# Kernel optimization log

Measured on AMD Instinct MI355X. Metric: run time of the kernel, lower is better.

Reference implementation:

```python
import jax, jax.numpy as jnp
import numpy as np

B, S, E, H = 2, 2048, 1024, 16
DH = E // H            # 64 head dim
ROT = DH // 2          # 32: RotaryEmbedding(head_dim//2) rotates first 32 dims only
CTX = 2048             # sliding KV window
THETA = 10000.0


def setup_inputs() -> dict:
    key = jax.random.key(0)
    ks = jax.random.split(key, 7)
    sc = 1.0 / np.sqrt(E)
    mk = lambda k, sh, s=1.0: (jax.random.normal(k, sh, jnp.float32) * s)
    return {
        "query": mk(ks[0], (B, S, E)),
        "key":   mk(ks[1], (B, S, E)),
        "value": mk(ks[2], (B, S, E)),
        "Wq": mk(ks[3], (E, E), sc), "bq": jnp.zeros((E,), jnp.float32),
        "Wk": mk(ks[4], (E, E), sc), "bk": jnp.zeros((E,), jnp.float32),
        "Wv": mk(ks[5], (E, E), sc), "bv": jnp.zeros((E,), jnp.float32),
        "Wo": mk(ks[6], (E, E), sc), "bo": jnp.zeros((E,), jnp.float32),
    }


def _rope(t):
    # t: [B, H, S, DH]; rotate first ROT dims, pass the rest through (offset=0).
    seq = t.shape[2]
    inv_freq = 1.0 / (THETA ** (jnp.arange(0, ROT, 2, dtype=jnp.float32) / ROT))  # [ROT//2]
    ang = jnp.arange(seq, dtype=jnp.float32)[:, None] * inv_freq[None, :]          # [S, ROT//2]
    cos = jnp.repeat(jnp.cos(ang), 2, axis=-1)  # [S, ROT] (pairwise-interleaved freqs)
    sin = jnp.repeat(jnp.sin(ang), 2, axis=-1)
    rot, rest = t[..., :ROT], t[..., ROT:]
    x1, x2 = rot[..., 0::2], rot[..., 1::2]
    rot_half = jnp.stack([-x2, x1], axis=-1).reshape(rot.shape)  # rotate_half on pairs
    return jnp.concatenate([rot * cos + rot_half * sin, rest], axis=-1)


def reference(query, key, value, Wq, bq, Wk, bk, Wv, bv, Wo, bo):
    def heads(x, W, b):
        return (x @ W.T + b).reshape(B, -1, H, DH).transpose(0, 2, 1, 3)  # [B,H,S,DH]

    q = _rope(heads(query, Wq, bq))
    k = _rope(heads(key, Wk, bk))
    v = heads(value, Wv, bv)
    k, v = k[:, :, -CTX:], v[:, :, -CTX:]  # sliding window (no-op when S == CTX)

    scale = jnp.float32(1.0 / np.sqrt(DH))
    scores = jnp.einsum('bhqd,bhkd->bhqk', q, k) * scale  # [B,H,Sq,Sk]
    sq, sk = q.shape[2], k.shape[2]
    causal = jnp.tril(jnp.ones((sk, sk), dtype=bool))[-sq:]  # [Sq,Sk]
    scores = jnp.where(causal[None, None], scores, jnp.float32(-jnp.inf))
    probs = jax.nn.softmax(scores, axis=-1)  # dropout=0 (eval)
    out = jnp.einsum('bhqk,bhkd->bhqd', probs, v)
    out = out.transpose(0, 2, 1, 3).reshape(B, -1, E)
    return out @ Wo.T + bo
```

## Files before the change

kernel.cpp:

```cpp
#include <hip/hip_runtime.h>
#include <stdint.h>
#include <math.h>

typedef __bf16 bf16x8 __attribute__((ext_vector_type(8)));
typedef float f32x4 __attribute__((ext_vector_type(4)));

__device__ __forceinline__ float bf2f(uint16_t x) {
  unsigned u = ((unsigned)x) << 16;
  float f;
  __builtin_memcpy(&f, &u, 4);
  return f;
}
__device__ __forceinline__ uint16_t f2bf(float f) {
  __bf16 h = (__bf16)f;
  uint16_t u;
  __builtin_memcpy(&u, &h, 2);
  return u;
}
__device__ __forceinline__ bf16x8 cvt8(const float* p) {
  const float4 lo = *(const float4*)p;
  const float4 hi = *(const float4*)(p + 4);
  bf16x8 v;
  v[0] = (__bf16)lo.x; v[1] = (__bf16)lo.y; v[2] = (__bf16)lo.z; v[3] = (__bf16)lo.w;
  v[4] = (__bf16)hi.x; v[5] = (__bf16)hi.y; v[6] = (__bf16)hi.z; v[7] = (__bf16)hi.w;
  return v;
}

typedef __attribute__((address_space(1))) const unsigned int gu32;
typedef __attribute__((address_space(3))) unsigned int lu32;
__device__ __forceinline__ void async_copy16(const void* gp, void* lp) {
  __builtin_amdgcn_global_load_lds((gu32*)gp, (lu32*)lp, 16, 0, 0);
}

__global__ __launch_bounds__(256) void cvt_kernel(
    const float* __restrict__ s0, uint16_t* __restrict__ d0,
    const float* __restrict__ s1, uint16_t* __restrict__ d1,
    const float* __restrict__ s2, uint16_t* __restrict__ d2) {
  const int z = blockIdx.z;
  const float* s = z == 0 ? s0 : z == 1 ? s1 : s2;
  uint16_t* d = z == 0 ? d0 : z == 1 ? d1 : d2;
  const size_t idx = ((size_t)blockIdx.x * 256 + threadIdx.x) * 8;
  *(bf16x8*)(d + idx) = cvt8(s + idx);
}

template <bool A_F32, bool W_F32, bool C_F32, bool VT, bool ROPE>
__global__ __launch_bounds__(256) void gemm3_kernel(
    const void* __restrict__ A0, const void* __restrict__ W0,
    const float* __restrict__ b0, void* __restrict__ C0,
    const void* __restrict__ A1, const void* __restrict__ W1,
    const float* __restrict__ b1, void* __restrict__ C1,
    const void* __restrict__ A2, const void* __restrict__ W2,
    const float* __restrict__ b2, void* __restrict__ C2,
    int M, int N, int K) {
  const int z = blockIdx.z;
  const void* Av = z == 0 ? A0 : z == 1 ? A1 : A2;
  const void* Wp = z == 0 ? W0 : z == 1 ? W1 : W2;
  const float* bias = z == 0 ? b0 : z == 1 ? b1 : b2;
  void* Cv = z == 0 ? C0 : z == 1 ? C1 : C2;

  __shared__ __align__(16) uint16_t As[128 * 64];
  __shared__ __align__(16) uint16_t Bs[64 * 64];
  const int tid = threadIdx.x;
  const int wave = tid >> 6, lane = tid & 63;
  const int quad = lane >> 4, l16 = lane & 15;
  const int l = blockIdx.y * 16 + blockIdx.x;
  const int bm = (l & 31) << 7;
  const int bn = (l >> 5) << 6;
  const int wm = (wave >> 1) << 6;
  const int wn = (wave & 1) << 5;

  f32x4 acc[4][2] = {};

  for (int k0 = 0; k0 < K; k0 += 64) {
    bf16x8 ar[4], wr[2];
    if (A_F32) {
#pragma unroll
      for (int i = 0; i < 4; i++) {
        const int c = i * 256 + tid;
        const int r = c >> 3, pc = ((c & 7) ^ (r & 7)) << 3;
        ar[i] = cvt8((const float*)Av + (size_t)(bm + r) * K + k0 + pc);
      }
    }
    if (W_F32) {
#pragma unroll
      for (int i = 0; i < 2; i++) {
        const int c = i * 256 + tid;
        const int r = c >> 3, pc = ((c & 7) ^ (r & 7)) << 3;
        wr[i] = cvt8((const float*)Wp + (size_t)(bn + r) * K + k0 + pc);
      }
    }
    if (k0) __syncthreads();
#pragma unroll
    for (int i = 0; i < 4; i++) {
      const int c = i * 256 + tid;
      const int r = c >> 3, pc = ((c & 7) ^ (r & 7)) << 3;
      if (A_F32) *(bf16x8*)(As + c * 8) = ar[i];
      else async_copy16((const uint16_t*)Av + (size_t)(bm + r) * K + k0 + pc,
                        As + (i * 256 + (tid & 192)) * 8);
    }
#pragma unroll
    for (int i = 0; i < 2; i++) {
      const int c = i * 256 + tid;
      const int r = c >> 3, pc = ((c & 7) ^ (r & 7)) << 3;
      if (W_F32) *(bf16x8*)(Bs + c * 8) = wr[i];
      else async_copy16((const uint16_t*)Wp + (size_t)(bn + r) * K + k0 + pc,
                        Bs + (i * 256 + (tid & 192)) * 8);
    }
    __syncthreads();
#pragma unroll
    for (int s = 0; s < 2; s++) {
      bf16x8 af[4], bfr[2];
#pragma unroll
      for (int i = 0; i < 4; i++) {
        const int Ra = wm + i * 16 + l16;
        af[i] = *(const bf16x8*)(As + Ra * 64 + (((s * 4 + quad) ^ (Ra & 7)) << 3));
      }
#pragma unroll
      for (int j = 0; j < 2; j++) {
        const int Rb = wn + j * 16 + l16;
        bfr[j] = *(const bf16x8*)(Bs + Rb * 64 + (((s * 4 + quad) ^ (Rb & 7)) << 3));
      }
#pragma unroll
      for (int i = 0; i < 4; i++)
#pragma unroll
        for (int j = 0; j < 2; j++)
          acc[i][j] = __builtin_amdgcn_mfma_f32_16x16x32_bf16(af[i], bfr[j], acc[i][j], 0, 0, 0);
    }
  }
  if (VT && z == 2) {
#pragma unroll
    for (int j = 0; j < 2; j++) {
      const int n = bn + wn + j * 16 + l16;
      const float bj = bias[n];
      const int h = n >> 6, dh = n & 63;
#pragma unroll
      for (int i = 0; i < 4; i++) {
        const int m0 = bm + wm + i * 16 + quad * 4;
        const int b = m0 >> 11, s0 = m0 & 2047;
        uint2 pk;
        pk.x = (unsigned)f2bf(acc[i][j][0] + bj) |
               ((unsigned)f2bf(acc[i][j][1] + bj) << 16);
        pk.y = (unsigned)f2bf(acc[i][j][2] + bj) |
               ((unsigned)f2bf(acc[i][j][3] + bj) << 16);
        *(uint2*)((uint16_t*)Cv + ((size_t)((b * 16 + h) * 64 + dh)) * 2048 + s0) = pk;
      }
    }
  } else {
#pragma unroll
    for (int j = 0; j < 2; j++) {
      const int n = bn + wn + j * 16 + l16;
      const float bj = bias[n];
      const int dh = wn + j * 16 + l16;
      const bool rot = ROPE && (wn == 0);
      float invrev = 0.f;
      if (rot)
        invrev = __expf(-0.5756462732485115f * (float)(dh >> 1)) *
                 0.15915494309189535f;
#pragma unroll
      for (int i = 0; i < 4; i++) {
        const int m0 = bm + wm + i * 16 + quad * 4;
#pragma unroll
        for (int r = 0; r < 4; r++) {
          float v = acc[i][j][r] + bj;
          if (rot) {
            const int s_pos = (m0 + r) & 2047;
            float rev = (float)s_pos * invrev;
            rev -= floorf(rev);
            const float sn = __builtin_amdgcn_sinf(rev);
            const float cs = __builtin_amdgcn_cosf(rev);
            const float partner = __shfl_xor(v, 1);
            v = (dh & 1) ? (v * cs + partner * sn) : (v * cs - partner * sn);
          }
          if (C_F32) ((float*)Cv)[(size_t)(m0 + r) * N + n] = v;
          else       ((uint16_t*)Cv)[(size_t)(m0 + r) * N + n] = f2bf(v);
        }
      }
    }
  }
}

__global__ __launch_bounds__(256) void flash_kernel(const uint16_t* __restrict__ Q,
                                                    const uint16_t* __restrict__ K,
                                                    const uint16_t* __restrict__ VT,
                                                    uint16_t* __restrict__ AO) {
  const int bx = blockIdx.x;
  const int xcd = bx & 7;
  const int slot = bx >> 3;
  const int bh = (slot >> 4) * 8 + xcd;
  const int qt2 = 15 - (slot & 15);
  const int h = bh & 15;
  const int b = bh >> 4;
  const int tid = threadIdx.x;
  const int wave = tid >> 6, lane = tid & 63;
  const int quad = lane >> 4, l16 = lane & 15;

  __shared__ __align__(16) uint16_t Ks[64 * 64];
  __shared__ __align__(16) uint16_t Vt[64 * 64];
  __shared__ __align__(16) uint16_t Ps[4][32 * 72];

  const int qrow0 = qt2 * 128 + wave * 16 + l16;
  const int qrow1 = qrow0 + 64;
  bf16x8 qf0[2], qf1[2];
#pragma unroll
  for (int s = 0; s < 2; s++) {
    union { bf16x8 v; uint16_t u[8]; } t0, t1;
    t0.v = *(const bf16x8*)(Q + ((size_t)(b * 2048 + qrow0) * 1024) + h * 64 + s * 32 + quad * 8);
    t1.v = *(const bf16x8*)(Q + ((size_t)(b * 2048 + qrow1) * 1024) + h * 64 + s * 32 + quad * 8);
#pragma unroll
    for (int j = 0; j < 8; j++) {
      t0.u[j] = f2bf(bf2f(t0.u[j]) * 0.125f);
      t1.u[j] = f2bf(bf2f(t1.u[j]) * 0.125f);
    }
    qf0[s] = t0.v;
    qf1[s] = t1.v;
  }

  const size_t vbase = ((size_t)((b * 16 + h) * 64)) * 2048;

  float lsum0 = 0.f, lsum1 = 0.f;
  f32x4 o0[4] = {}, o1[4] = {};

  const int nkt = 2 * qt2 + 2;
  for (int kt = 0; kt < nkt; kt++) {
    if (kt) __syncthreads();
#pragma unroll
    for (int i = 0; i < 2; i++) {
      const int c = i * 256 + tid;
      const int r = c >> 3, pc = ((c & 7) ^ (r & 7)) << 3;
      async_copy16(K + ((size_t)(b * 2048 + kt * 64 + r) * 1024) + h * 64 + pc,
                   Ks + (i * 256 + (tid & 192)) * 8);
      async_copy16(VT + vbase + (size_t)r * 2048 + kt * 64 + pc,
                   Vt + (i * 256 + (tid & 192)) * 8);
    }
    __syncthreads();

    const bool f0 = (kt < nkt - 1);

    {
      f32x4 sacc[4] = {};
#pragma unroll
      for (int s = 0; s < 2; s++)
#pragma unroll
        for (int t = 0; t < 4; t++) {
          const int R = t * 16 + l16;
          bf16x8 kf = *(const bf16x8*)(Ks + R * 64 + (((s * 4 + quad) ^ (R & 7)) << 3));
          sacc[t] = __builtin_amdgcn_mfma_f32_16x16x32_bf16(kf, qf1[s], sacc[t], 0, 0, 0);
        }
      if (kt == nkt - 1) {
#pragma unroll
        for (int t = 0; t < 4; t++)
#pragma unroll
          for (int r = 0; r < 4; r++)
            if (kt * 64 + t * 16 + quad * 4 + r > qrow1) sacc[t][r] = -1e30f;
      }
#pragma unroll
      for (int t = 0; t < 4; t++) {
        float p0 = __expf(sacc[t][0]), p1 = __expf(sacc[t][1]);
        float p2 = __expf(sacc[t][2]), p3 = __expf(sacc[t][3]);
        lsum1 += (p0 + p1) + (p2 + p3);
        uint2 pk;
        pk.x = (unsigned)f2bf(p0) | ((unsigned)f2bf(p1) << 16);
        pk.y = (unsigned)f2bf(p2) | ((unsigned)f2bf(p3) << 16);
        *(uint2*)(&Ps[wave][(16 + l16) * 72 + t * 16 + quad * 4]) = pk;
      }
    }
    if (f0) {
      f32x4 sacc[4] = {};
#pragma unroll
      for (int s = 0; s < 2; s++)
#pragma unroll
        for (int t = 0; t < 4; t++) {
          const int R = t * 16 + l16;
          bf16x8 kf = *(const bf16x8*)(Ks + R * 64 + (((s * 4 + quad) ^ (R & 7)) << 3));
          sacc[t] = __builtin_amdgcn_mfma_f32_16x16x32_bf16(kf, qf0[s], sacc[t], 0, 0, 0);
        }
      if (kt == nkt - 2) {
#pragma unroll
        for (int t = 0; t < 4; t++)
#pragma unroll
          for (int r = 0; r < 4; r++)
            if (kt * 64 + t * 16 + quad * 4 + r > qrow0) sacc[t][r] = -1e30f;
      }
#pragma unroll
      for (int t = 0; t < 4; t++) {
        float p0 = __expf(sacc[t][0]), p1 = __expf(sacc[t][1]);
        float p2 = __expf(sacc[t][2]), p3 = __expf(sacc[t][3]);
        lsum0 += (p0 + p1) + (p2 + p3);
        uint2 pk;
        pk.x = (unsigned)f2bf(p0) | ((unsigned)f2bf(p1) << 16);
        pk.y = (unsigned)f2bf(p2) | ((unsigned)f2bf(p3) << 16);
        *(uint2*)(&Ps[wave][l16 * 72 + t * 16 + quad * 4]) = pk;
      }
    }
#pragma unroll
    for (int s = 0; s < 2; s++) {
      const bf16x8 pa1 = *(const bf16x8*)(&Ps[wave][(16 + l16) * 72 + s * 32 + quad * 8]);
#pragma unroll
      for (int t = 0; t < 4; t++) {
        const int R = t * 16 + l16;
        const bf16x8 vb = *(const bf16x8*)(Vt + R * 64 + (((s * 4 + quad) ^ (R & 7)) << 3));
        o1[t] = __builtin_amdgcn_mfma_f32_16x16x32_bf16(pa1, vb, o1[t], 0, 0, 0);
      }
    }
    if (f0) {
#pragma unroll
      for (int s = 0; s < 2; s++) {
        const bf16x8 pa0 = *(const bf16x8*)(&Ps[wave][l16 * 72 + s * 32 + quad * 8]);
#pragma unroll
        for (int t = 0; t < 4; t++) {
          const int R = t * 16 + l16;
          const bf16x8 vb = *(const bf16x8*)(Vt + R * 64 + (((s * 4 + quad) ^ (R & 7)) << 3));
          o0[t] = __builtin_amdgcn_mfma_f32_16x16x32_bf16(pa0, vb, o0[t], 0, 0, 0);
        }
      }
    }
  }
  lsum0 += __shfl_xor(lsum0, 16);
  lsum0 += __shfl_xor(lsum0, 32);
  lsum1 += __shfl_xor(lsum1, 16);
  lsum1 += __shfl_xor(lsum1, 32);
  const float inv0 = 1.f / lsum0, inv1 = 1.f / lsum1;
  float invr0[4], invr1[4];
#pragma unroll
  for (int r = 0; r < 4; r++) {
    invr0[r] = __shfl(inv0, quad * 4 + r);
    invr1[r] = __shfl(inv1, quad * 4 + r);
  }
#pragma unroll
  for (int t = 0; t < 4; t++)
#pragma unroll
    for (int r = 0; r < 4; r++) {
      const int qg0 = qt2 * 128 + wave * 16 + quad * 4 + r;
      AO[((size_t)(b * 2048 + qg0) * 1024) + h * 64 + t * 16 + l16] =
          f2bf(o0[t][r] * invr0[r]);
      AO[((size_t)(b * 2048 + qg0 + 64) * 1024) + h * 64 + t * 16 + l16] =
          f2bf(o1[t][r] * invr1[r]);
    }
}

extern "C" void kernel_launch(void* const* d_in, const int* in_sizes, int n_in,
                              void* d_out, int out_size, void* d_ws, size_t ws_size,
                              hipStream_t stream) {
  const float* query = (const float*)d_in[0];
  const float* key   = (const float*)d_in[1];
  const float* value = (const float*)d_in[2];
  const float* Wq = (const float*)d_in[3];
  const float* bq = (const float*)d_in[4];
  const float* Wk = (const float*)d_in[5];
  const float* bk = (const float*)d_in[6];
  const float* Wv = (const float*)d_in[7];
  const float* bv = (const float*)d_in[8];
  const float* Wo = (const float*)d_in[9];
  const float* bo = (const float*)d_in[10];
  float* out = (float*)d_out;

  uint16_t* ws = (uint16_t*)d_ws;
  uint16_t* Qb  = ws;
  uint16_t* Kb  = ws + (size_t)4194304;
  uint16_t* VTb = ws + (size_t)8388608;
  uint16_t* AOb = ws + (size_t)12582912;
  uint16_t* Wqc = AOb;
  uint16_t* Wkc = AOb + (size_t)1048576;
  uint16_t* Wvc = AOb + (size_t)2097152;

  dim3 blk(256);
  cvt_kernel<<<dim3(512, 1, 3), blk, 0, stream>>>(Wq, Wqc, Wk, Wkc, Wv, Wvc);
  gemm3_kernel<true, false, false, true, true><<<dim3(16, 32, 3), blk, 0, stream>>>(
      query, Wqc, bq, Qb,
      key,   Wkc, bk, Kb,
      value, Wvc, bv, VTb,
      4096, 1024, 1024);
  flash_kernel<<<dim3(512), blk, 0, stream>>>(Qb, Kb, VTb, AOb);
  gemm3_kernel<false, true, true, false, false><<<dim3(16, 32, 1), blk, 0, stream>>>(
      AOb, Wo, bo, out,
      AOb, Wo, bo, out,
      AOb, Wo, bo, out,
      4096, 1024, 1024);
}
```

Measured before the change: 243.1 us.

## Widen QKV GEMM tile to 128 columns and prefetch fp32 operands a step ahead

After: 250.8 us. 1.03x slower.

```diff
diff --git a/kernel.cpp b/kernel.cpp
--- a/kernel.cpp
+++ b/kernel.cpp
@@ -43,7 +43,7 @@
   *(bf16x8*)(d + idx) = cvt8(s + idx);
 }
 
-template <bool A_F32, bool W_F32, bool C_F32, bool VT, bool ROPE>
+template <bool A_F32, bool W_F32, bool C_F32, bool VT, bool ROPE, int NF>
 __global__ __launch_bounds__(256) void gemm3_kernel(
     const void* __restrict__ A0, const void* __restrict__ W0,
     const float* __restrict__ b0, void* __restrict__ C0,
@@ -52,6 +52,7 @@
     const void* __restrict__ A2, const void* __restrict__ W2,
     const float* __restrict__ b2, void* __restrict__ C2,
     int M, int N, int K) {
+  constexpr int BN = NF * 32;
   const int z = blockIdx.z;
   const void* Av = z == 0 ? A0 : z == 1 ? A1 : A2;
   const void* Wp = z == 0 ? W0 : z == 1 ? W1 : W2;
@@ -59,77 +60,109 @@
   void* Cv = z == 0 ? C0 : z == 1 ? C1 : C2;
 
   __shared__ __align__(16) uint16_t As[128 * 64];
-  __shared__ __align__(16) uint16_t Bs[64 * 64];
+  __shared__ __align__(16) uint16_t Bs[BN * 64];
   const int tid = threadIdx.x;
   const int wave = tid >> 6, lane = tid & 63;
   const int quad = lane >> 4, l16 = lane & 15;
-  const int l = blockIdx.y * 16 + blockIdx.x;
+  const int l = blockIdx.y * gridDim.x + blockIdx.x;
   const int bm = (l & 31) << 7;
-  const int bn = (l >> 5) << 6;
+  const int bn = (l >> 5) * BN;
   const int wm = (wave >> 1) << 6;
-  const int wn = (wave & 1) << 5;
-
-  f32x4 acc[4][2] = {};
+  const int wn = (wave & 1) * (BN / 2);
+
+  f32x4 acc[4][NF] = {};
+  bf16x8 ar[4], wr[NF];
+
+  if (A_F32) {
+#pragma unroll
+    for (int i = 0; i < 4; i++) {
+      const int c = i * 256 + tid;
+      const int r = c >> 3, pc = ((c & 7) ^ (r & 7)) << 3;
+      ar[i] = cvt8((const float*)Av + (size_t)(bm + r) * K + pc);
+    }
+  }
+  if (W_F32) {
+#pragma unroll
+    for (int i = 0; i < NF; i++) {
+      const int c = i * 256 + tid;
+      const int r = c >> 3, pc = ((c & 7) ^ (r & 7)) << 3;
+      wr[i] = cvt8((const float*)Wp + (size_t)(bn + r) * K + pc);
+    }
+  }
 
   for (int k0 = 0; k0 < K; k0 += 64) {
-    bf16x8 ar[4], wr[2];
-    if (A_F32) {
+    if (k0) __syncthreads();
+    if (!A_F32) {
 #pragma unroll
       for (int i = 0; i < 4; i++) {
         const int c = i * 256 + tid;
         const int r = c >> 3, pc = ((c & 7) ^ (r & 7)) << 3;
-        ar[i] = cvt8((const float*)Av + (size_t)(bm + r) * K + k0 + pc);
-      }
-    }
-    if (W_F32) {
-#pragma unroll
-      for (int i = 0; i < 2; i++) {
+        async_copy16((const uint16_t*)Av + (size_t)(bm + r) * K + k0 + pc,
+                     As + (i * 256 + (tid & 192)) * 8);
+      }
+    }
+    if (!W_F32) {
+#pragma unroll
+      for (int i = 0; i < NF; i++) {
         const int c = i * 256 + tid;
         const int r = c >> 3, pc = ((c & 7) ^ (r & 7)) << 3;
-        wr[i] = cvt8((const float*)Wp + (size_t)(bn + r) * K + k0 + pc);
-      }
-    }
-    if (k0) __syncthreads();
-#pragma unroll
-    for (int i = 0; i < 4; i++) {
-      const int c = i * 256 + tid;
-      const int r = c >> 3, pc = ((c & 7) ^ (r & 7)) << 3;
-      if (A_F32) *(bf16x8*)(As + c * 8) = ar[i];
-      else async_copy16((const uint16_t*)Av + (size_t)(bm + r) * K + k0 + pc,
-                        As + (i * 256 + (tid & 192)) * 8);
-    }
-#pragma unroll
-    for (int i = 0; i < 2; i++) {
-      const int c = i * 256 + tid;
-      const int r = c >> 3, pc = ((c & 7) ^ (r & 7)) << 3;
-      if (W_F32) *(bf16x8*)(Bs + c * 8) = wr[i];
-      else async_copy16((const uint16_t*)Wp + (size_t)(bn + r) * K + k0 + pc,
-                        Bs + (i * 256 + (tid & 192)) * 8);
+        async_copy16((const uint16_t*)Wp + (size_t)(bn + r) * K + k0 + pc,
+                     Bs + (i * 256 + (tid & 192)) * 8);
+      }
+    }
+    if (A_F32) {
+#pragma unroll
+      for (int i = 0; i < 4; i++)
+        *(bf16x8*)(As + (i * 256 + tid) * 8) = ar[i];
+    }
+    if (W_F32) {
+#pragma unroll
+      for (int i = 0; i < NF; i++)
+        *(bf16x8*)(Bs + (i * 256 + tid) * 8) = wr[i];
     }
     __syncthreads();
+    const int kn = k0 + 64;
+    if (kn < K) {
+      if (A_F32) {
+#pragma unroll
+        for (int i = 0; i < 4; i++) {
+          const int c = i * 256 + tid;
+          const int r = c >> 3, pc = ((c & 7) ^ (r & 7)) << 3;
+          ar[i] = cvt8((const float*)Av + (size_t)(bm + r) * K + kn + pc);
+        }
+      }
+      if (W_F32) {
+#pragma unroll
+        for (int i = 0; i < NF; i++) {
+          const int c = i * 256 + tid;
+          const int r = c >> 3, pc = ((c & 7) ^ (r & 7)) << 3;
+          wr[i] = cvt8((const float*)Wp + (size_t)(bn + r) * K + kn + pc);
+        }
+      }
+    }
 #pragma unroll
     for (int s = 0; s < 2; s++) {
-      bf16x8 af[4], bfr[2];
+      bf16x8 af[4], bfr[NF];
 #pragma unroll
       for (int i = 0; i < 4; i++) {
         const int Ra = wm + i * 16 + l16;
         af[i] = *(const bf16x8*)(As + Ra * 64 + (((s * 4 + quad) ^ (Ra & 7)) << 3));
       }
 #pragma unroll
-      for (int j = 0; j < 2; j++) {
+      for (int j = 0; j < NF; j++) {
         const int Rb = wn + j * 16 + l16;
         bfr[j] = *(const bf16x8*)(Bs + Rb * 64 + (((s * 4 + quad) ^ (Rb & 7)) << 3));
       }
 #pragma unroll
       for (int i = 0; i < 4; i++)
 #pragma unroll
-        for (int j = 0; j < 2; j++)
+        for (int j = 0; j < NF; j++)
           acc[i][j] = __builtin_amdgcn_mfma_f32_16x16x32_bf16(af[i], bfr[j], acc[i][j], 0, 0, 0);
     }
   }
   if (VT && z == 2) {
 #pragma unroll
-    for (int j = 0; j < 2; j++) {
+    for (int j = 0; j < NF; j++) {
       const int n = bn + wn + j * 16 + l16;
       const float bj = bias[n];
       const int h = n >> 6, dh = n & 63;
@@ -147,11 +180,11 @@
     }
   } else {
 #pragma unroll
-    for (int j = 0; j < 2; j++) {
+    for (int j = 0; j < NF; j++) {
       const int n = bn + wn + j * 16 + l16;
       const float bj = bias[n];
-      const int dh = wn + j * 16 + l16;
-      const bool rot = ROPE && (wn == 0);
+      const int dh = (wn + j * 16 + l16) & 63;
+      const bool rot = ROPE && (((wn + j * 16) & 63) < 32);
       float invrev = 0.f;
       if (rot)
         invrev = __expf(-0.5756462732485115f * (float)(dh >> 1)) *
@@ -365,13 +398,13 @@
 
   dim3 blk(256);
   cvt_kernel<<<dim3(512, 1, 3), blk, 0, stream>>>(Wq, Wqc, Wk, Wkc, Wv, Wvc);
-  gemm3_kernel<true, false, false, true, true><<<dim3(16, 32, 3), blk, 0, stream>>>(
+  gemm3_kernel<true, false, false, true, true, 4><<<dim3(8, 32, 3), blk, 0, stream>>>(
       query, Wqc, bq, Qb,
       key,   Wkc, bk, Kb,
       value, Wvc, bv, VTb,
       4096, 1024, 1024);
   flash_kernel<<<dim3(512), blk, 0, stream>>>(Qb, Kb, VTb, AOb);
-  gemm3_kernel<false, true, true, false, false><<<dim3(16, 32, 1), blk, 0, stream>>>(
+  gemm3_kernel<false, true, true, false, false, 2><<<dim3(16, 32, 1), blk, 0, stream>>>(
       AOb, Wo, bo, out,
       AOb, Wo, bo, out,
       AOb, Wo, bo, out,
```
